# Kernel optimization log

Measured on AMD Instinct MI355X. Metric: run time of the kernel, lower is better.

The kernel has to match this reference:

```python
import jax, jax.numpy as jnp
import numpy as np

NUM_EDGE_TYPES = 38
NUM_NODE_TYPES = 4
HIDDEN = 64
HOPS = 4
N_NODES = 100_000
N_EDGES = 1_600_000


def setup_inputs() -> dict:
    key = jax.random.key(0)
    ks = jax.random.split(key, 7)
    in_dim = NUM_EDGE_TYPES + 2 * NUM_NODE_TYPES  # 46
    return {
        "edge_index": jax.random.randint(ks[0], (2, N_EDGES), 0, N_NODES),
        "edge_type": jax.random.randint(ks[1], (N_EDGES,), 0, NUM_EDGE_TYPES),
        "node_type": jax.random.randint(ks[2], (N_NODES,), 0, NUM_NODE_TYPES),
        "W1": jax.random.normal(ks[3], (in_dim, HIDDEN), dtype=jnp.float32) * 0.1,
        "b1": jax.random.normal(ks[4], (HIDDEN,), dtype=jnp.float32) * 0.1,
        "W2": jax.random.normal(ks[5], (HIDDEN, 1), dtype=jnp.float32) * 0.1,
        "b2": jax.random.normal(ks[6], (1,), dtype=jnp.float32) * 0.1,
    }


def reference(edge_index, edge_type, node_type, W1, b1, W2, b2):
    src, dst = edge_index[0], edge_index[1]  # PyG: x_j = x[edge_index[0]], aggregate at edge_index[1]
    head_type = node_type[src]
    tail_type = node_type[dst]
    # Linear over concat of three one-hots == sum of three gathered weight rows + bias.
    h = (W1[edge_type]
         + W1[NUM_EDGE_TYPES + head_type]
         + W1[NUM_EDGE_TYPES + NUM_NODE_TYPES + tail_type]
         + b1)                                   # [E, HIDDEN]
    h = jax.nn.gelu(h)
    edge_emb = jax.nn.sigmoid(h @ W2 + b2)       # [E, 1]

    num_nodes = node_type.shape[0]
    aggr = jnp.zeros((num_nodes, 1), dtype=edge_emb.dtype)
    for _ in range(HOPS):
        msg = aggr[src] + edge_emb               # gather + add, [E, 1]
        aggr = jax.ops.segment_sum(msg, dst, num_segments=num_nodes)  # scatter-add
    return aggr
```

## Files before the change

### kernel.cpp

```cpp
#include <hip/hip_runtime.h>

#define NUM_EDGE_TYPES 38
#define NUM_NODE_TYPES 4
#define HIDDEN 64
#define TABLE_SIZE (NUM_EDGE_TYPES * NUM_NODE_TYPES * NUM_NODE_TYPES)
#define SRC_BITS 17
#define SRC_MASK ((1 << SRC_BITS) - 1)
#define BSHIFT 8
#define BNODES 256
#define MAXB 512
#define PB 512
#define CHUNK (PB * 8)
#define HB 1024
#define CAPC 6144

__device__ __forceinline__ float table_entry(int i, const float* __restrict__ W1,
                                             const float* __restrict__ b1,
                                             const float* __restrict__ W2,
                                             const float* __restrict__ b2) {
    int et = i >> 4, ht = (i >> 2) & 3, tt = i & 3;
    const float* r0 = W1 + et * HIDDEN;
    const float* r1 = W1 + (NUM_EDGE_TYPES + ht) * HIDDEN;
    const float* r2 = W1 + (NUM_EDGE_TYPES + NUM_NODE_TYPES + tt) * HIDDEN;
    float acc = b2[0];
#pragma unroll 8
    for (int k = 0; k < HIDDEN; ++k) {
        float h = r0[k] + r1[k] + r2[k] + b1[k];
        float u = 0.7978845608028654f * (h + 0.044715f * h * h * h);
        float g = 0.5f * h * (1.0f + tanhf(u));
        acc += g * W2[k];
    }
    return 1.0f / (1.0f + expf(-acc));
}

__global__ void init_kernel(const float* __restrict__ W1, const float* __restrict__ b1,
                            const float* __restrict__ W2, const float* __restrict__ b2,
                            float* __restrict__ table, int* __restrict__ cursor) {
    int t = threadIdx.x;
    if (t < MAXB) cursor[t] = 0;
    if (t < TABLE_SIZE) table[t] = table_entry(t, W1, b1, W2, b2);
}

__global__ void table_kernel(const float* __restrict__ W1, const float* __restrict__ b1,
                             const float* __restrict__ W2, const float* __restrict__ b2,
                             float* __restrict__ table) {
    int i = blockIdx.x * blockDim.x + threadIdx.x;
    if (i < TABLE_SIZE) table[i] = table_entry(i, W1, b1, W2, b2);
}

__global__ void partition_kernel(const int* __restrict__ src, const int* __restrict__ dst,
                                 const int* __restrict__ etype, int* __restrict__ cursor,
                                 int* __restrict__ pack, int E, int nbk, int cap) {
    __shared__ int hist[MAXB];
    __shared__ int locCur[MAXB];
    for (int i = threadIdx.x; i < nbk; i += PB) hist[i] = 0;
    __syncthreads();
    int start = blockIdx.x * CHUNK;
    int end = min(start + CHUNK, E);
    if (end - start == CHUNK) {
        int j0 = start + threadIdx.x * 4;
        int j1 = start + PB * 4 + threadIdx.x * 4;
        int4 da = *(const int4*)(dst + j0);
        int4 db = *(const int4*)(dst + j1);
        atomicAdd(&hist[da.x >> BSHIFT], 1);
        atomicAdd(&hist[da.y >> BSHIFT], 1);
        atomicAdd(&hist[da.z >> BSHIFT], 1);
        atomicAdd(&hist[da.w >> BSHIFT], 1);
        atomicAdd(&hist[db.x >> BSHIFT], 1);
        atomicAdd(&hist[db.y >> BSHIFT], 1);
        atomicAdd(&hist[db.z >> BSHIFT], 1);
        atomicAdd(&hist[db.w >> BSHIFT], 1);
        int4 sa = *(const int4*)(src + j0);
        int4 sb = *(const int4*)(src + j1);
        int4 ea = *(const int4*)(etype + j0);
        int4 eb = *(const int4*)(etype + j1);
        __syncthreads();
        for (int i = threadIdx.x; i < nbk; i += PB) {
            int h = hist[i];
            locCur[i] = h ? i * cap + atomicAdd(&cursor[i], h) : 0;
        }
        __syncthreads();
        int t0 = atomicAdd(&locCur[da.x >> BSHIFT], 1);
        int t1 = atomicAdd(&locCur[da.y >> BSHIFT], 1);
        int t2 = atomicAdd(&locCur[da.z >> BSHIFT], 1);
        int t3 = atomicAdd(&locCur[da.w >> BSHIFT], 1);
        int t4 = atomicAdd(&locCur[db.x >> BSHIFT], 1);
        int t5 = atomicAdd(&locCur[db.y >> BSHIFT], 1);
        int t6 = atomicAdd(&locCur[db.z >> BSHIFT], 1);
        int t7 = atomicAdd(&locCur[db.w >> BSHIFT], 1);
        pack[t0] = (ea.x << (SRC_BITS + 8)) | ((da.x & (BNODES - 1)) << SRC_BITS) | sa.x;
        pack[t1] = (ea.y << (SRC_BITS + 8)) | ((da.y & (BNODES - 1)) << SRC_BITS) | sa.y;
        pack[t2] = (ea.z << (SRC_BITS + 8)) | ((da.z & (BNODES - 1)) << SRC_BITS) | sa.z;
        pack[t3] = (ea.w << (SRC_BITS + 8)) | ((da.w & (BNODES - 1)) << SRC_BITS) | sa.w;
        pack[t4] = (eb.x << (SRC_BITS + 8)) | ((db.x & (BNODES - 1)) << SRC_BITS) | sb.x;
        pack[t5] = (eb.y << (SRC_BITS + 8)) | ((db.y & (BNODES - 1)) << SRC_BITS) | sb.y;
        pack[t6] = (eb.z << (SRC_BITS + 8)) | ((db.z & (BNODES - 1)) << SRC_BITS) | sb.z;
        pack[t7] = (eb.w << (SRC_BITS + 8)) | ((db.w & (BNODES - 1)) << SRC_BITS) | sb.w;
    } else {
        for (int j = start + threadIdx.x; j < end; j += PB)
            atomicAdd(&hist[dst[j] >> BSHIFT], 1);
        __syncthreads();
        for (int i = threadIdx.x; i < nbk; i += PB) {
            int h = hist[i];
            locCur[i] = h ? i * cap + atomicAdd(&cursor[i], h) : 0;
        }
        __syncthreads();
        for (int j = start + threadIdx.x; j < end; j += PB) {
            int d = dst[j];
            int slot = atomicAdd(&locCur[d >> BSHIFT], 1);
            pack[slot] = (etype[j] << (SRC_BITS + 8)) | ((d & (BNODES - 1)) << SRC_BITS) | src[j];
        }
    }
}

__global__ void sort_base_kernel(int* __restrict__ pack, const int* __restrict__ cursor,
                                 const int* __restrict__ ntype, const float* __restrict__ table,
                                 float* __restrict__ base, int* __restrict__ nodeOffG,
                                 int N, int cap) {
    __shared__ int rawL[CAPC];
    __shared__ int sortedL[CAPC];
    __shared__ float tbl[TABLE_SIZE];
    __shared__ int nodeCnt[BNODES];
    __shared__ int nodeOff[BNODES + 1];
    __shared__ unsigned char ntLoc[BNODES];
    int b = blockIdx.x;
    int node0 = b << BSHIFT;
    int tid = threadIdx.x;
    int st = b * cap;
    int c = min(cursor[b], cap);

    if (tid < TABLE_SIZE) tbl[tid] = table[tid];
    if (tid < BNODES) {
        nodeCnt[tid] = 0;
        int n = node0 + tid;
        ntLoc[tid] = (n < N) ? (unsigned char)ntype[n] : 0;
    }
    __syncthreads();

    int c4 = c & ~3;
    for (int j = tid * 4; j < c4; j += HB * 4) {
        int4 v = *(const int4*)(pack + st + j);
        *(int4*)(rawL + j) = v;
        atomicAdd(&nodeCnt[(v.x >> SRC_BITS) & (BNODES - 1)], 1);
        atomicAdd(&nodeCnt[(v.y >> SRC_BITS) & (BNODES - 1)], 1);
        atomicAdd(&nodeCnt[(v.z >> SRC_BITS) & (BNODES - 1)], 1);
        atomicAdd(&nodeCnt[(v.w >> SRC_BITS) & (BNODES - 1)], 1);
    }
    for (int j = c4 + tid; j < c; j += HB) {
        int p = pack[st + j];
        rawL[j] = p;
        atomicAdd(&nodeCnt[(p >> SRC_BITS) & (BNODES - 1)], 1);
    }
    __syncthreads();

    if (tid < 64) {
        int lane = tid;
        int v0 = nodeCnt[lane * 4], v1 = nodeCnt[lane * 4 + 1];
        int v2 = nodeCnt[lane * 4 + 2], v3 = nodeCnt[lane * 4 + 3];
        int s = v0 + v1 + v2 + v3;
        int inc = s;
        for (int d = 1; d < 64; d <<= 1) {
            int t = __shfl_up(inc, d, 64);
            if (lane >= d) inc += t;
        }
        int excl = inc - s;
        nodeOff[lane * 4]     = excl;
        nodeOff[lane * 4 + 1] = excl + v0;
        nodeOff[lane * 4 + 2] = excl + v0 + v1;
        nodeOff[lane * 4 + 3] = excl + v0 + v1 + v2;
        if (lane == 63) nodeOff[BNODES] = inc;
    }
    __syncthreads();
    if (tid < BNODES) nodeCnt[tid] = 0;
    __syncthreads();

    {
        int j = tid;
        for (; j + HB < c; j += 2 * HB) {
            int p0 = rawL[j];
            int p1 = rawL[j + HB];
            int dl0 = (p0 >> SRC_BITS) & (BNODES - 1);
            int dl1 = (p1 >> SRC_BITS) & (BNODES - 1);
            int r0 = atomicAdd(&nodeCnt[dl0], 1);
            int r1 = atomicAdd(&nodeCnt[dl1], 1);
            sortedL[nodeOff[dl0] + r0] = p0;
            sortedL[nodeOff[dl1] + r1] = p1;
        }
        if (j < c) {
            int p = rawL[j];
            int dl = (p >> SRC_BITS) & (BNODES - 1);
            int r = atomicAdd(&nodeCnt[dl], 1);
            sortedL[nodeOff[dl] + r] = p;
        }
    }
    __syncthreads();

    for (int j = tid * 4; j < c4; j += HB * 4)
        *(int4*)(pack + st + j) = *(const int4*)(sortedL + j);
    for (int j = c4 + tid; j < c; j += HB) pack[st + j] = sortedL[j];
    if (tid < BNODES) nodeOffG[(b << BSHIFT) + tid] = nodeOff[tid];

    int node = tid >> 2, l = tid & 3;
    int lo = nodeOff[node], hi = nodeOff[node + 1];
    int nt = ntLoc[node];
    float s = 0.0f;
    int j = lo + l;
    for (; j + 4 < hi; j += 8) {
        int p0 = sortedL[j], p1 = sortedL[j + 4];
        s += tbl[((((unsigned)p0) >> (SRC_BITS + 8)) << 4) | (ntype[p0 & SRC_MASK] << 2) | nt]
           + tbl[((((unsigned)p1) >> (SRC_BITS + 8)) << 4) | (ntype[p1 & SRC_MASK] << 2) | nt];
    }
    if (j < hi) {
        int p = sortedL[j];
        s += tbl[((((unsigned)p) >> (SRC_BITS + 8)) << 4) | (ntype[p & SRC_MASK] << 2) | nt];
    }
    s += __shfl_xor(s, 1, 64);
    s += __shfl_xor(s, 2, 64);
    int n = node0 + node;
    if (l == 0 && n < N) base[n] = s;
}

__global__ __launch_bounds__(512)
void hop_csr_kernel(const int* __restrict__ pack, const int* __restrict__ nodeOffG,
                    const int* __restrict__ cursor, const float* __restrict__ base,
                    const float* __restrict__ prev, float* __restrict__ out,
                    int N, int cap) {
    __shared__ int off[129];
    int blk = blockIdx.x;
    int b = blk >> 1;
    int half = blk & 1;
    int tid = threadIdx.x;
    int st = b * cap;
    int nodeBase = (b << BSHIFT) + half * 128;
    if (tid < 128) off[tid] = nodeOffG[(b << BSHIFT) + half * 128 + tid];
    else if (tid == 128)
        off[128] = half ? min(cursor[b], cap) : nodeOffG[(b << BSHIFT) + 128];
    __syncthreads();
    int node = tid >> 2, l = tid & 3;
    int lo = off[node], hi = off[node + 1];
    float s = 0.0f;
    int j = st + lo + l;
    int hiG = st + hi;
    for (; j + 12 < hiG; j += 16) {
        int p0 = pack[j], p1 = pack[j + 4], p2 = pack[j + 8], p3 = pack[j + 12];
        s += prev[p0 & SRC_MASK] + prev[p1 & SRC_MASK]
           + prev[p2 & SRC_MASK] + prev[p3 & SRC_MASK];
    }
    for (; j < hiG; j += 4) s += prev[pack[j] & SRC_MASK];
    s += __shfl_xor(s, 1, 64);
    s += __shfl_xor(s, 2, 64);
    int n = nodeBase + node;
    if (l == 0 && n < N) out[n] = base[n] + s;
}

__global__ void edge_base_kernel(const int* __restrict__ src, const int* __restrict__ dst,
                                 const int* __restrict__ etype, const int* __restrict__ ntype,
                                 const float* __restrict__ table, float* __restrict__ base, int E) {
    __shared__ float tbl[TABLE_SIZE];
    for (int i = threadIdx.x; i < TABLE_SIZE; i += blockDim.x) tbl[i] = table[i];
    __syncthreads();
    int e = blockIdx.x * blockDim.x + threadIdx.x;
    if (e >= E) return;
    int s = src[e];
    int d = dst[e];
    int idx = (etype[e] << 4) | (ntype[s] << 2) | ntype[d];
    atomicAdd(base + d, tbl[idx]);
}

__global__ void copy_kernel(const float* __restrict__ in, float* __restrict__ out, int N) {
    int i = blockIdx.x * blockDim.x + threadIdx.x;
    if (i < N) out[i] = in[i];
}

__global__ void edge_hop_kernel(const int* __restrict__ src, const int* __restrict__ dst,
                                const float* __restrict__ prev, float* __restrict__ next, int E) {
    int e = blockIdx.x * blockDim.x + threadIdx.x;
    if (e >= E) return;
    atomicAdd(next + dst[e], prev[src[e]]);
}

extern "C" void kernel_launch(void* const* d_in, const int* in_sizes, int n_in,
                              void* d_out, int out_size, void* d_ws, size_t ws_size,
                              hipStream_t stream) {
    const int* edge_index = (const int*)d_in[0];
    const int* etype      = (const int*)d_in[1];
    const int* ntype      = (const int*)d_in[2];
    const float* W1       = (const float*)d_in[3];
    const float* b1       = (const float*)d_in[4];
    const float* W2       = (const float*)d_in[5];
    const float* b2       = (const float*)d_in[6];

    const int E = in_sizes[1];
    const int N = in_sizes[2];
    const int* src = edge_index;
    const int* dst = edge_index + E;
    float* out = (float*)d_out;

    const int nbk = (N + BNODES - 1) >> BSHIFT;
    const int nChunks = (E + CHUNK - 1) / CHUNK;

    int cap = ((E / (nbk > 0 ? nbk : 1)) * 3 / 2 + 255) & ~255;
    if (cap < 512) cap = 512;
    size_t packElems = (size_t)nbk * cap;

    size_t need = (packElems + MAXB + (size_t)nbk * BNODES + 1024 + (size_t)3 * N) * 4 + 256;

    if (ws_size >= need && nbk <= MAXB && cap <= CAPC) {
        int* pack     = (int*)d_ws;
        int* cursor   = pack + packElems;
        int* nodeOffG = cursor + MAXB;
        float* table  = (float*)(nodeOffG + (size_t)nbk * BNODES);
        float* base   = table + 1024;
        float* bufA   = base + N;
        float* bufB   = bufA + N;

        init_kernel<<<1, 1024, 0, stream>>>(W1, b1, W2, b2, table, cursor);
        partition_kernel<<<nChunks, PB, 0, stream>>>(src, dst, etype, cursor, pack, E, nbk, cap);
        sort_base_kernel<<<nbk, HB, 0, stream>>>(pack, cursor, ntype, table, base, nodeOffG, N, cap);
        hop_csr_kernel<<<2 * nbk, 512, 0, stream>>>(pack, nodeOffG, cursor, base, base, bufA, N, cap);
        hop_csr_kernel<<<2 * nbk, 512, 0, stream>>>(pack, nodeOffG, cursor, base, bufA, bufB, N, cap);
        hop_csr_kernel<<<2 * nbk, 512, 0, stream>>>(pack, nodeOffG, cursor, base, bufB, out, N, cap);
    } else {
        float* table = (float*)d_ws;
        float* base  = table + 1024;
        float* bufA  = base + N;
        float* bufB  = bufA + N;
        const int eb = (E + 255) / 256;
        const int nb = (N + 255) / 256;

        hipMemsetAsync(base, 0, (size_t)N * sizeof(float), stream);
        table_kernel<<<(TABLE_SIZE + 255) / 256, 256, 0, stream>>>(W1, b1, W2, b2, table);

        edge_base_kernel<<<eb, 256, 0, stream>>>(src, dst, etype, ntype, table, base, E);
        copy_kernel<<<nb, 256, 0, stream>>>(base, bufA, N);
        edge_hop_kernel<<<eb, 256, 0, stream>>>(src, dst, base, bufA, E);
        copy_kernel<<<nb, 256, 0, stream>>>(base, bufB, N);
        edge_hop_kernel<<<eb, 256, 0, stream>>>(src, dst, bufA, bufB, E);
        copy_kernel<<<nb, 256, 0, stream>>>(base, out, N);
        edge_hop_kernel<<<eb, 256, 0, stream>>>(src, dst, bufB, out, E);
    }
}
```

Baseline: 147.2 us.

## Replace per-bucket CSR sort with LDS atomic accumulation in base and hop kernels

Removes the in-block counting sort that built per-node CSR offsets. The base and hop kernels now stream each bucket's packed edges and accumulate into a 256-entry shared-memory array with float atomics. This drops the sort's shared-memory passes, the write-back of sorted edges and the node-offset array, but adds LDS atomic contention. Hop kernels also launch half as many blocks (one per bucket), so there is less parallelism. Floating-point summation order becomes nondeterministic.

```diff
diff --git a/kernel.cpp b/kernel.cpp
--- a/kernel.cpp
+++ b/kernel.cpp
@@ -11,7 +11,6 @@
 #define MAXB 512
 #define PB 512
 #define CHUNK (PB * 8)
-#define HB 1024
 #define CAPC 6144
 
 __device__ __forceinline__ float table_entry(int i, const float* __restrict__ W1,
@@ -113,144 +112,89 @@
     }
 }
 
-__global__ void sort_base_kernel(int* __restrict__ pack, const int* __restrict__ cursor,
-                                 const int* __restrict__ ntype, const float* __restrict__ table,
-                                 float* __restrict__ base, int* __restrict__ nodeOffG,
-                                 int N, int cap) {
-    __shared__ int rawL[CAPC];
-    __shared__ int sortedL[CAPC];
+__global__ __launch_bounds__(512)
+void base_lds_kernel(const int* __restrict__ pack, const int* __restrict__ cursor,
+                     const int* __restrict__ ntype, const float* __restrict__ table,
+                     float* __restrict__ base, int N, int cap) {
     __shared__ float tbl[TABLE_SIZE];
-    __shared__ int nodeCnt[BNODES];
-    __shared__ int nodeOff[BNODES + 1];
+    __shared__ float accL[BNODES];
     __shared__ unsigned char ntLoc[BNODES];
     int b = blockIdx.x;
+    int tid = threadIdx.x;
     int node0 = b << BSHIFT;
-    int tid = threadIdx.x;
     int st = b * cap;
     int c = min(cursor[b], cap);
 
-    if (tid < TABLE_SIZE) tbl[tid] = table[tid];
+    for (int i = tid; i < TABLE_SIZE; i += 512) tbl[i] = table[i];
     if (tid < BNODES) {
-        nodeCnt[tid] = 0;
+        accL[tid] = 0.0f;
         int n = node0 + tid;
-        ntLoc[tid] = (n < N) ? (unsigned char)ntype[n] : 0;
+        ntLoc[tid] = (n < N) ? (unsigned char)ntype[n] : (unsigned char)0;
     }
     __syncthreads();
 
     int c4 = c & ~3;
-    for (int j = tid * 4; j < c4; j += HB * 4) {
+    for (int j = tid * 4; j < c4; j += 512 * 4) {
         int4 v = *(const int4*)(pack + st + j);
-        *(int4*)(rawL + j) = v;
-        atomicAdd(&nodeCnt[(v.x >> SRC_BITS) & (BNODES - 1)], 1);
-        atomicAdd(&nodeCnt[(v.y >> SRC_BITS) & (BNODES - 1)], 1);
-        atomicAdd(&nodeCnt[(v.z >> SRC_BITS) & (BNODES - 1)], 1);
-        atomicAdd(&nodeCnt[(v.w >> SRC_BITS) & (BNODES - 1)], 1);
-    }
-    for (int j = c4 + tid; j < c; j += HB) {
+        int s0 = v.x & SRC_MASK, s1 = v.y & SRC_MASK;
+        int s2 = v.z & SRC_MASK, s3 = v.w & SRC_MASK;
+        int h0 = ntype[s0], h1 = ntype[s1], h2 = ntype[s2], h3 = ntype[s3];
+        int d0 = (v.x >> SRC_BITS) & (BNODES - 1);
+        int d1 = (v.y >> SRC_BITS) & (BNODES - 1);
+        int d2 = (v.z >> SRC_BITS) & (BNODES - 1);
+        int d3 = (v.w >> SRC_BITS) & (BNODES - 1);
+        atomicAdd(&accL[d0], tbl[(int)((((unsigned)v.x) >> (SRC_BITS + 8)) << 4) | (h0 << 2) | (int)ntLoc[d0]]);
+        atomicAdd(&accL[d1], tbl[(int)((((unsigned)v.y) >> (SRC_BITS + 8)) << 4) | (h1 << 2) | (int)ntLoc[d1]]);
+        atomicAdd(&accL[d2], tbl[(int)((((unsigned)v.z) >> (SRC_BITS + 8)) << 4) | (h2 << 2) | (int)ntLoc[d2]]);
+        atomicAdd(&accL[d3], tbl[(int)((((unsigned)v.w) >> (SRC_BITS + 8)) << 4) | (h3 << 2) | (int)ntLoc[d3]]);
+    }
+    for (int j = c4 + tid; j < c; j += 512) {
         int p = pack[st + j];
-        rawL[j] = p;
-        atomicAdd(&nodeCnt[(p >> SRC_BITS) & (BNODES - 1)], 1);
-    }
-    __syncthreads();
-
-    if (tid < 64) {
-        int lane = tid;
-        int v0 = nodeCnt[lane * 4], v1 = nodeCnt[lane * 4 + 1];
-        int v2 = nodeCnt[lane * 4 + 2], v3 = nodeCnt[lane * 4 + 3];
-        int s = v0 + v1 + v2 + v3;
-        int inc = s;
-        for (int d = 1; d < 64; d <<= 1) {
-            int t = __shfl_up(inc, d, 64);
-            if (lane >= d) inc += t;
-        }
-        int excl = inc - s;
-        nodeOff[lane * 4]     = excl;
-        nodeOff[lane * 4 + 1] = excl + v0;
-        nodeOff[lane * 4 + 2] = excl + v0 + v1;
-        nodeOff[lane * 4 + 3] = excl + v0 + v1 + v2;
-        if (lane == 63) nodeOff[BNODES] = inc;
-    }
-    __syncthreads();
-    if (tid < BNODES) nodeCnt[tid] = 0;
-    __syncthreads();
-
-    {
-        int j = tid;
-        for (; j + HB < c; j += 2 * HB) {
-            int p0 = rawL[j];
-            int p1 = rawL[j + HB];
-            int dl0 = (p0 >> SRC_BITS) & (BNODES - 1);
-            int dl1 = (p1 >> SRC_BITS) & (BNODES - 1);
-            int r0 = atomicAdd(&nodeCnt[dl0], 1);
-            int r1 = atomicAdd(&nodeCnt[dl1], 1);
-            sortedL[nodeOff[dl0] + r0] = p0;
-            sortedL[nodeOff[dl1] + r1] = p1;
-        }
-        if (j < c) {
-            int p = rawL[j];
-            int dl = (p >> SRC_BITS) & (BNODES - 1);
-            int r = atomicAdd(&nodeCnt[dl], 1);
-            sortedL[nodeOff[dl] + r] = p;
-        }
-    }
-    __syncthreads();
-
-    for (int j = tid * 4; j < c4; j += HB * 4)
-        *(int4*)(pack + st + j) = *(const int4*)(sortedL + j);
-    for (int j = c4 + tid; j < c; j += HB) pack[st + j] = sortedL[j];
-    if (tid < BNODES) nodeOffG[(b << BSHIFT) + tid] = nodeOff[tid];
-
-    int node = tid >> 2, l = tid & 3;
-    int lo = nodeOff[node], hi = nodeOff[node + 1];
-    int nt = ntLoc[node];
-    float s = 0.0f;
-    int j = lo + l;
-    for (; j + 4 < hi; j += 8) {
-        int p0 = sortedL[j], p1 = sortedL[j + 4];
-        s += tbl[((((unsigned)p0) >> (SRC_BITS + 8)) << 4) | (ntype[p0 & SRC_MASK] << 2) | nt]
-           + tbl[((((unsigned)p1) >> (SRC_BITS + 8)) << 4) | (ntype[p1 & SRC_MASK] << 2) | nt];
-    }
-    if (j < hi) {
-        int p = sortedL[j];
-        s += tbl[((((unsigned)p) >> (SRC_BITS + 8)) << 4) | (ntype[p & SRC_MASK] << 2) | nt];
-    }
-    s += __shfl_xor(s, 1, 64);
-    s += __shfl_xor(s, 2, 64);
-    int n = node0 + node;
-    if (l == 0 && n < N) base[n] = s;
+        int dl = (p >> SRC_BITS) & (BNODES - 1);
+        int h = ntype[p & SRC_MASK];
+        atomicAdd(&accL[dl], tbl[(int)((((unsigned)p) >> (SRC_BITS + 8)) << 4) | (h << 2) | (int)ntLoc[dl]]);
+    }
+    __syncthreads();
+    if (tid < BNODES) {
+        int n = node0 + tid;
+        if (n < N) base[n] = accL[tid];
+    }
 }
 
 __global__ __launch_bounds__(512)
-void hop_csr_kernel(const int* __restrict__ pack, const int* __restrict__ nodeOffG,
-                    const int* __restrict__ cursor, const float* __restrict__ base,
-                    const float* __restrict__ prev, float* __restrict__ out,
-                    int N, int cap) {
-    __shared__ int off[129];
-    int blk = blockIdx.x;
-    int b = blk >> 1;
-    int half = blk & 1;
+void hop_lds_kernel(const int* __restrict__ pack, const int* __restrict__ cursor,
+                    const float* __restrict__ base, const float* __restrict__ prev,
+                    float* __restrict__ out, int N, int cap) {
+    __shared__ float accL[BNODES];
+    int b = blockIdx.x;
     int tid = threadIdx.x;
+    int node0 = b << BSHIFT;
     int st = b * cap;
-    int nodeBase = (b << BSHIFT) + half * 128;
-    if (tid < 128) off[tid] = nodeOffG[(b << BSHIFT) + half * 128 + tid];
-    else if (tid == 128)
-        off[128] = half ? min(cursor[b], cap) : nodeOffG[(b << BSHIFT) + 128];
-    __syncthreads();
-    int node = tid >> 2, l = tid & 3;
-    int lo = off[node], hi = off[node + 1];
-    float s = 0.0f;
-    int j = st + lo + l;
-    int hiG = st + hi;
-    for (; j + 12 < hiG; j += 16) {
-        int p0 = pack[j], p1 = pack[j + 4], p2 = pack[j + 8], p3 = pack[j + 12];
-        s += prev[p0 & SRC_MASK] + prev[p1 & SRC_MASK]
-           + prev[p2 & SRC_MASK] + prev[p3 & SRC_MASK];
-    }
-    for (; j < hiG; j += 4) s += prev[pack[j] & SRC_MASK];
-    s += __shfl_xor(s, 1, 64);
-    s += __shfl_xor(s, 2, 64);
-    int n = nodeBase + node;
-    if (l == 0 && n < N) out[n] = base[n] + s;
+    int c = min(cursor[b], cap);
+    if (tid < BNODES) accL[tid] = 0.0f;
+    __syncthreads();
+
+    int c4 = c & ~3;
+    for (int j = tid * 4; j < c4; j += 512 * 4) {
+        int4 v = *(const int4*)(pack + st + j);
+        float g0 = prev[v.x & SRC_MASK];
+        float g1 = prev[v.y & SRC_MASK];
+        float g2 = prev[v.z & SRC_MASK];
+        float g3 = prev[v.w & SRC_MASK];
+        atomicAdd(&accL[(v.x >> SRC_BITS) & (BNODES - 1)], g0);
+        atomicAdd(&accL[(v.y >> SRC_BITS) & (BNODES - 1)], g1);
+        atomicAdd(&accL[(v.z >> SRC_BITS) & (BNODES - 1)], g2);
+        atomicAdd(&accL[(v.w >> SRC_BITS) & (BNODES - 1)], g3);
+    }
+    for (int j = c4 + tid; j < c; j += 512) {
+        int p = pack[st + j];
+        atomicAdd(&accL[(p >> SRC_BITS) & (BNODES - 1)], prev[p & SRC_MASK]);
+    }
+    __syncthreads();
+    if (tid < BNODES) {
+        int n = node0 + tid;
+        if (n < N) out[n] = base[n] + accL[tid];
+    }
 }
 
 __global__ void edge_base_kernel(const int* __restrict__ src, const int* __restrict__ dst,
@@ -303,23 +247,22 @@
     if (cap < 512) cap = 512;
     size_t packElems = (size_t)nbk * cap;
 
-    size_t need = (packElems + MAXB + (size_t)nbk * BNODES + 1024 + (size_t)3 * N) * 4 + 256;
+    size_t need = (packElems + MAXB + 1024 + (size_t)3 * N) * 4 + 256;
 
     if (ws_size >= need && nbk <= MAXB && cap <= CAPC) {
         int* pack     = (int*)d_ws;
         int* cursor   = pack + packElems;
-        int* nodeOffG = cursor + MAXB;
-        float* table  = (float*)(nodeOffG + (size_t)nbk * BNODES);
+        float* table  = (float*)(cursor + MAXB);
         float* base   = table + 1024;
         float* bufA   = base + N;
         float* bufB   = bufA + N;
 
         init_kernel<<<1, 1024, 0, stream>>>(W1, b1, W2, b2, table, cursor);
         partition_kernel<<<nChunks, PB, 0, stream>>>(src, dst, etype, cursor, pack, E, nbk, cap);
-        sort_base_kernel<<<nbk, HB, 0, stream>>>(pack, cursor, ntype, table, base, nodeOffG, N, cap);
-        hop_csr_kernel<<<2 * nbk, 512, 0, stream>>>(pack, nodeOffG, cursor, base, base, bufA, N, cap);
-        hop_csr_kernel<<<2 * nbk, 512, 0, stream>>>(pack, nodeOffG, cursor, base, bufA, bufB, N, cap);
-        hop_csr_kernel<<<2 * nbk, 512, 0, stream>>>(pack, nodeOffG, cursor, base, bufB, out, N, cap);
+        base_lds_kernel<<<nbk, 512, 0, stream>>>(pack, cursor, ntype, table, base, N, cap);
+        hop_lds_kernel<<<nbk, 512, 0, stream>>>(pack, cursor, base, base, bufA, N, cap);
+        hop_lds_kernel<<<nbk, 512, 0, stream>>>(pack, cursor, base, bufA, bufB, N, cap);
+        hop_lds_kernel<<<nbk, 512, 0, stream>>>(pack, cursor, base, bufB, out, N, cap);
     } else {
         float* table = (float*)d_ws;
         float* base  = table + 1024;
```

Result: slower. 157.3 us (+6.9%).

## Fold table build into partition kernel and split hop blocks into quarters

Applied to the files above, without the earlier changes.

Removes the single-block init kernel, zeroes the cursor with a memset instead, and computes the 608-entry edge-embedding table inside the first eight partition blocks, with one wavefront per entry and a shuffle reduction over the 64 hidden units. The hop kernel now launches four blocks per 256-node bucket and assigns eight lanes to each node instead of four. This is meant to drop the serial per-thread init launch from the critical path and to spread the gather work over more blocks and lanes. The cost is extra tail work in a few partition blocks and more idle lanes on nodes with few edges.

```diff
diff --git a/kernel.cpp b/kernel.cpp
--- a/kernel.cpp
+++ b/kernel.cpp
@@ -33,14 +33,6 @@
     return 1.0f / (1.0f + expf(-acc));
 }
 
-__global__ void init_kernel(const float* __restrict__ W1, const float* __restrict__ b1,
-                            const float* __restrict__ W2, const float* __restrict__ b2,
-                            float* __restrict__ table, int* __restrict__ cursor) {
-    int t = threadIdx.x;
-    if (t < MAXB) cursor[t] = 0;
-    if (t < TABLE_SIZE) table[t] = table_entry(t, W1, b1, W2, b2);
-}
-
 __global__ void table_kernel(const float* __restrict__ W1, const float* __restrict__ b1,
                              const float* __restrict__ W2, const float* __restrict__ b2,
                              float* __restrict__ table) {
@@ -50,7 +42,10 @@
 
 __global__ void partition_kernel(const int* __restrict__ src, const int* __restrict__ dst,
                                  const int* __restrict__ etype, int* __restrict__ cursor,
-                                 int* __restrict__ pack, int E, int nbk, int cap) {
+                                 int* __restrict__ pack, int E, int nbk, int cap,
+                                 const float* __restrict__ W1, const float* __restrict__ b1,
+                                 const float* __restrict__ W2, const float* __restrict__ b2,
+                                 float* __restrict__ table) {
     __shared__ int hist[MAXB];
     __shared__ int locCur[MAXB];
     for (int i = threadIdx.x; i < nbk; i += PB) hist[i] = 0;
@@ -111,6 +106,29 @@
             pack[slot] = (etype[j] << (SRC_BITS + 8)) | ((d & (BNODES - 1)) << SRC_BITS) | src[j];
         }
     }
+
+    for (int seg = blockIdx.x; seg < 8; seg += gridDim.x) {
+        int wid = threadIdx.x >> 6, lane = threadIdx.x & 63;
+        int e0 = seg * 76;
+        int e1 = min(e0 + 76, TABLE_SIZE);
+        for (int e = e0 + wid; e < e1; e += PB / 64) {
+            int et = e >> 4, ht = (e >> 2) & 3, tt = e & 3;
+            float h = W1[et * HIDDEN + lane]
+                    + W1[(NUM_EDGE_TYPES + ht) * HIDDEN + lane]
+                    + W1[(NUM_EDGE_TYPES + NUM_NODE_TYPES + tt) * HIDDEN + lane]
+                    + b1[lane];
+            float u = 0.7978845608028654f * (h + 0.044715f * h * h * h);
+            float g = 0.5f * h * (1.0f + tanhf(u));
+            float v = g * W2[lane];
+            v += __shfl_xor(v, 32, 64);
+            v += __shfl_xor(v, 16, 64);
+            v += __shfl_xor(v, 8, 64);
+            v += __shfl_xor(v, 4, 64);
+            v += __shfl_xor(v, 2, 64);
+            v += __shfl_xor(v, 1, 64);
+            if (lane == 0) table[e] = 1.0f / (1.0f + expf(-(v + b2[0])));
+        }
+    }
 }
 
 __global__ void sort_base_kernel(int* __restrict__ pack, const int* __restrict__ cursor,
@@ -225,30 +243,30 @@
                     const int* __restrict__ cursor, const float* __restrict__ base,
                     const float* __restrict__ prev, float* __restrict__ out,
                     int N, int cap) {
-    __shared__ int off[129];
+    __shared__ int off[65];
     int blk = blockIdx.x;
-    int b = blk >> 1;
-    int half = blk & 1;
+    int b = blk >> 2;
+    int q = blk & 3;
     int tid = threadIdx.x;
     int st = b * cap;
-    int nodeBase = (b << BSHIFT) + half * 128;
-    if (tid < 128) off[tid] = nodeOffG[(b << BSHIFT) + half * 128 + tid];
-    else if (tid == 128)
-        off[128] = half ? min(cursor[b], cap) : nodeOffG[(b << BSHIFT) + 128];
-    __syncthreads();
-    int node = tid >> 2, l = tid & 3;
+    int nodeBase = (b << BSHIFT) + q * 64;
+    if (tid < 64) off[tid] = nodeOffG[nodeBase + tid];
+    else if (tid == 64)
+        off[64] = (q == 3) ? min(cursor[b], cap) : nodeOffG[nodeBase + 64];
+    __syncthreads();
+    int node = tid >> 3, l = tid & 7;
     int lo = off[node], hi = off[node + 1];
     float s = 0.0f;
     int j = st + lo + l;
     int hiG = st + hi;
-    for (; j + 12 < hiG; j += 16) {
-        int p0 = pack[j], p1 = pack[j + 4], p2 = pack[j + 8], p3 = pack[j + 12];
-        s += prev[p0 & SRC_MASK] + prev[p1 & SRC_MASK]
-           + prev[p2 & SRC_MASK] + prev[p3 & SRC_MASK];
-    }
-    for (; j < hiG; j += 4) s += prev[pack[j] & SRC_MASK];
+    for (; j + 8 < hiG; j += 16) {
+        int p0 = pack[j], p1 = pack[j + 8];
+        s += prev[p0 & SRC_MASK] + prev[p1 & SRC_MASK];
+    }
+    if (j < hiG) s += prev[pack[j] & SRC_MASK];
     s += __shfl_xor(s, 1, 64);
     s += __shfl_xor(s, 2, 64);
+    s += __shfl_xor(s, 4, 64);
     int n = nodeBase + node;
     if (l == 0 && n < N) out[n] = base[n] + s;
 }
@@ -314,12 +332,13 @@
         float* bufA   = base + N;
         float* bufB   = bufA + N;
 
-        init_kernel<<<1, 1024, 0, stream>>>(W1, b1, W2, b2, table, cursor);
-        partition_kernel<<<nChunks, PB, 0, stream>>>(src, dst, etype, cursor, pack, E, nbk, cap);
+        hipMemsetAsync(cursor, 0, MAXB * sizeof(int), stream);
+        partition_kernel<<<nChunks, PB, 0, stream>>>(src, dst, etype, cursor, pack, E, nbk, cap,
+                                                     W1, b1, W2, b2, table);
         sort_base_kernel<<<nbk, HB, 0, stream>>>(pack, cursor, ntype, table, base, nodeOffG, N, cap);
-        hop_csr_kernel<<<2 * nbk, 512, 0, stream>>>(pack, nodeOffG, cursor, base, base, bufA, N, cap);
-        hop_csr_kernel<<<2 * nbk, 512, 0, stream>>>(pack, nodeOffG, cursor, base, bufA, bufB, N, cap);
-        hop_csr_kernel<<<2 * nbk, 512, 0, stream>>>(pack, nodeOffG, cursor, base, bufB, out, N, cap);
+        hop_csr_kernel<<<4 * nbk, 512, 0, stream>>>(pack, nodeOffG, cursor, base, base, bufA, N, cap);
+        hop_csr_kernel<<<4 * nbk, 512, 0, stream>>>(pack, nodeOffG, cursor, base, bufA, bufB, N, cap);
+        hop_csr_kernel<<<4 * nbk, 512, 0, stream>>>(pack, nodeOffG, cursor, base, bufB, out, N, cap);
     } else {
         float* table = (float*)d_ws;
         float* base  = table + 1024;
```

New measurement: 136.4 us. 1.08x faster.
